# Kernel tuning notes

Measured on AMD Instinct MI355X. Metric: run time of the kernel, lower is better.

## Reference

```python
import jax, jax.numpy as jnp
import numpy as np

B, N, C, Q, H, RATIO = 8, 8700, 256, 300, 8, 4
D = C // H
HID = C * RATIO
EPS = 1e-5


def _ln(x, w, b):
    m = jnp.mean(x, axis=-1, keepdims=True)
    v = jnp.mean((x - m) ** 2, axis=-1, keepdims=True)
    return (x - m) * jax.lax.rsqrt(v + EPS) * w + b


def setup_inputs() -> dict:
    key = jax.random.key(0)
    ks = jax.random.split(key, 8)
    s = 0.02
    return {
        "x": jax.random.normal(ks[0], (B, N, C), jnp.float32),
        # linear weights stored [in, out] (y = x @ W), no biases (qkv_bias=False, Mlp bias=False)
        "Wq": jax.random.normal(ks[1], (C, C), jnp.float32) * s,
        "Wk": jax.random.normal(ks[2], (C, C), jnp.float32) * s,
        "Wv": jax.random.normal(ks[3], (C, C), jnp.float32) * s,
        "Wp": jax.random.normal(ks[4], (C, C), jnp.float32) * s,
        "W1": jax.random.normal(ks[5], (C, HID), jnp.float32) * s,
        "W2": jax.random.normal(ks[6], (HID, C), jnp.float32) * s,
        "ln1_w": jnp.ones((C,), jnp.float32),
        "ln1_b": jnp.zeros((C,), jnp.float32),
        "ln2_w": jnp.ones((C,), jnp.float32),
        "ln2_b": jnp.zeros((C,), jnp.float32),
        "gamma1": jnp.ones((C,), jnp.float32),
        "gamma2": jnp.ones((C,), jnp.float32),
    }


def reference(x, Wq, Wk, Wv, Wp, W1, W2, ln1_w, ln1_b, ln2_w, ln2_b, gamma1, gamma2):
    scale = D ** -0.5
    xn = _ln(x, ln1_w, ln1_b)                       # [B,N,C]
    # SAQAttn: queries only from the first Q tokens; keys/values from all N tokens
    q = (xn[:, :Q] @ Wq).reshape(B, Q, H, D) * scale  # [B,Q,H,D]
    k = (xn @ Wk).reshape(B, N, H, D)
    v = (xn @ Wv).reshape(B, N, H, D)
    attn = jax.nn.softmax(jnp.einsum('bqhd,bnhd->bhqn', q, k), axis=-1)  # [B,H,Q,N]
    x_det = jnp.einsum('bhqn,bnhd->bqhd', attn, v).reshape(B, Q, C) @ Wp  # [B,Q,C]
    # residual with layer-scale gamma1; context tokens pass normed features through
    x_attn = jnp.concatenate([x_det, xn[:, Q:]], axis=1)
    x = x + gamma1 * x_attn
    # tokens_norm=False: norm2 only on query tokens
    x = jnp.concatenate([_ln(x[:, :Q], ln2_w, ln2_b), x[:, Q:]], axis=1)
    # MLP on query tokens with layer-scale gamma2 (exact GELU, as nn.GELU default)
    det = gamma2 * (jax.nn.gelu(x[:, :Q] @ W1, approximate=False) @ W2)
    # faithful to source: x_res + cat([det, x[:,Q:]]) doubles the context tokens
    return x + jnp.concatenate([det, x[:, Q:]], axis=1)
```

## Files before the change

kernel.cpp:

```cpp
#include <hip/hip_runtime.h>

#define BB 8
#define NN 8700
#define CC 256
#define QQ 300
#define HH 8
#define DD 32
#define HIDN 1024
#define NSPLIT 16
#define TSTR (NSPLIT * 64)
#define KSLACK 1536

typedef unsigned short u16;
typedef __attribute__((ext_vector_type(8))) short short8;
typedef __attribute__((ext_vector_type(4))) float f32x4;

#define MFMA16(a, b, c) __builtin_amdgcn_mfma_f32_16x16x32_bf16((a), (b), (c), 0, 0, 0)

__device__ __forceinline__ u16 f2bu(float f) {
    unsigned int u = __builtin_bit_cast(unsigned int, f);
    u += 0x7fffu + ((u >> 16) & 1u);
    return (u16)(u >> 16);
}
__device__ __forceinline__ unsigned int cvtpk(float lo, float hi) {
    unsigned int r;
    asm("v_cvt_pk_bf16_f32 %0, %1, %2" : "=v"(r) : "v"(lo), "v"(hi));
    return r;
}

__global__ __launch_bounds__(256)
void wprep_all(const float* __restrict__ Wq, const float* __restrict__ Wk,
               const float* __restrict__ Wv, const float* __restrict__ Wp,
               const float* __restrict__ W1, const float* __restrict__ W2,
               u16* __restrict__ dst, float qscale)
{
    int e = blockIdx.x * 256 + threadIdx.x;
    float v;
    if (e < 65536)       { int i = e;          int n = i >> 8, k = i & 255;   v = Wq[k * 256 + n] * qscale; }
    else if (e < 131072) { int i = e - 65536;  int n = i >> 8, k = i & 255;   v = Wk[k * 256 + n]; }
    else if (e < 196608) { int i = e - 131072; int n = i >> 8, k = i & 255;   v = Wv[k * 256 + n]; }
    else if (e < 262144) { int i = e - 196608; int n = i >> 8, k = i & 255;   v = Wp[k * 256 + n]; }
    else if (e < 524288) { int i = e - 262144; int n = i >> 8, k = i & 255;   v = W1[k * 1024 + n]; }
    else                 { int i = e - 524288; int n = i >> 10, k = i & 1023; v = W2[k * 256 + n]; }
    dst[e] = f2bu(v);
}

__global__ __launch_bounds__(256)
void ln1_k(const float* __restrict__ x, const float* __restrict__ w,
           const float* __restrict__ bv, const float* __restrict__ g1,
           u16* __restrict__ xn, float* __restrict__ out)
{
    int row = blockIdx.x * 4 + (threadIdx.x >> 6);
    int l = threadIdx.x & 63;
    size_t base = (size_t)row * CC + l * 4;
    float4 xv = *reinterpret_cast<const float4*>(x + base);
    float s  = xv.x + xv.y + xv.z + xv.w;
    float s2 = xv.x * xv.x + xv.y * xv.y + xv.z * xv.z + xv.w * xv.w;
#pragma unroll
    for (int m = 1; m < 64; m <<= 1) {
        s  += __shfl_xor(s,  m, 64);
        s2 += __shfl_xor(s2, m, 64);
    }
    float mean = s * (1.0f / CC);
    float rs = rsqrtf(s2 * (1.0f / CC) - mean * mean + 1e-5f);
    float4 wv = *reinterpret_cast<const float4*>(w  + l * 4);
    float4 bb = *reinterpret_cast<const float4*>(bv + l * 4);
    float n0 = (xv.x - mean) * rs * wv.x + bb.x;
    float n1 = (xv.y - mean) * rs * wv.y + bb.y;
    float n2 = (xv.z - mean) * rs * wv.z + bb.z;
    float n3 = (xv.w - mean) * rs * wv.w + bb.w;
    ushort4 u; u.x = f2bu(n0); u.y = f2bu(n1); u.z = f2bu(n2); u.w = f2bu(n3);
    *reinterpret_cast<ushort4*>(xn + base) = u;
    int n = row % NN;
    if (n >= QQ) {
        float4 gv = *reinterpret_cast<const float4*>(g1 + l * 4);
        float4 o;
        o.x = 2.0f * (xv.x + gv.x * n0);
        o.y = 2.0f * (xv.y + gv.y * n1);
        o.z = 2.0f * (xv.z + gv.z * n2);
        o.w = 2.0f * (xv.w + gv.w * n3);
        *reinterpret_cast<float4*>(out + base) = o;
    }
}

__global__ __launch_bounds__(256)
void ln2_k(const float* __restrict__ x, const float* __restrict__ pd,
           const float* __restrict__ g1, const float* __restrict__ w,
           const float* __restrict__ bv, float* __restrict__ xqf, u16* __restrict__ xqb)
{
    int r = blockIdx.x * 4 + (threadIdx.x >> 6);
    int l = threadIdx.x & 63;
    int b = r / QQ, n = r - b * QQ;
    size_t xoff = ((size_t)b * NN + n) * CC + l * 4;
    size_t roff = (size_t)r * CC + l * 4;
    float4 xv = *reinterpret_cast<const float4*>(x + xoff);
    float4 pv = *reinterpret_cast<const float4*>(pd + roff);
    float4 gv = *reinterpret_cast<const float4*>(g1 + l * 4);
    float x0 = xv.x + gv.x * pv.x;
    float x1 = xv.y + gv.y * pv.y;
    float x2 = xv.z + gv.z * pv.z;
    float x3 = xv.w + gv.w * pv.w;
    float s  = x0 + x1 + x2 + x3;
    float s2 = x0 * x0 + x1 * x1 + x2 * x2 + x3 * x3;
#pragma unroll
    for (int m = 1; m < 64; m <<= 1) {
        s  += __shfl_xor(s,  m, 64);
        s2 += __shfl_xor(s2, m, 64);
    }
    float mean = s * (1.0f / CC);
    float rs = rsqrtf(s2 * (1.0f / CC) - mean * mean + 1e-5f);
    float4 wv = *reinterpret_cast<const float4*>(w  + l * 4);
    float4 bb = *reinterpret_cast<const float4*>(bv + l * 4);
    float n0 = (x0 - mean) * rs * wv.x + bb.x;
    float n1 = (x1 - mean) * rs * wv.y + bb.y;
    float n2 = (x2 - mean) * rs * wv.z + bb.z;
    float n3 = (x3 - mean) * rs * wv.w + bb.w;
    float4 o; o.x = n0; o.y = n1; o.z = n2; o.w = n3;
    *reinterpret_cast<float4*>(xqf + roff) = o;
    ushort4 u; u.x = f2bu(n0); u.y = f2bu(n1); u.z = f2bu(n2); u.w = f2bu(n3);
    *reinterpret_cast<ushort4*>(xqb + roff) = u;
}

template<int EPI, int MT>
__global__ __launch_bounds__(256)
void gemm_k(const u16* __restrict__ A, const u16* __restrict__ WT,
            u16* __restrict__ Cb, u16* __restrict__ Cb2, float* __restrict__ Cf,
            const float* __restrict__ basep, const float* __restrict__ gvec,
            float* __restrict__ outp,
            int M, int K, int ldC, int rpb, int bstr)
{
    constexpr int NM = MT / 16;
    const int w = threadIdx.x >> 6, l = threadIdx.x & 63;
    const int l15 = l & 15, kg = l >> 4;
    const int rowbase = blockIdx.x * MT;
    const int colbase = blockIdx.y * 256 + w * 64;
    const short8 z8 = {0, 0, 0, 0, 0, 0, 0, 0};
    const f32x4 fz = {0.f, 0.f, 0.f, 0.f};

    const u16* ap[NM]; bool av[NM];
#pragma unroll
    for (int mi = 0; mi < NM; mi++) {
        int r = rowbase + mi * 16 + l15;
        av[mi] = (r < M);
        int rr = av[mi] ? r : 0;
        size_t ar = (size_t)(rr / rpb) * bstr + (rr % rpb);
        ap[mi] = A + ar * K + kg * 8;
    }
    const u16* bp[4];
#pragma unroll
    for (int ni = 0; ni < 4; ni++) {
        int col = colbase + ni * 16 + l15;
        bp[ni] = WT + (size_t)col * K + kg * 8;
    }
    f32x4 acc[NM][4];
#pragma unroll
    for (int mi = 0; mi < NM; mi++)
#pragma unroll
        for (int ni = 0; ni < 4; ni++) acc[mi][ni] = fz;

    for (int ks = 0; ks < K; ks += 32) {
        short8 a[NM], bfr[4];
#pragma unroll
        for (int mi = 0; mi < NM; mi++)
            a[mi] = av[mi] ? *reinterpret_cast<const short8*>(ap[mi] + ks) : z8;
#pragma unroll
        for (int ni = 0; ni < 4; ni++)
            bfr[ni] = *reinterpret_cast<const short8*>(bp[ni] + ks);
#pragma unroll
        for (int mi = 0; mi < NM; mi++)
#pragma unroll
            for (int ni = 0; ni < 4; ni++)
                acc[mi][ni] = MFMA16(a[mi], bfr[ni], acc[mi][ni]);
    }
#pragma unroll
    for (int mi = 0; mi < NM; mi++) {
#pragma unroll
        for (int j = 0; j < 4; j++) {
            int r = rowbase + mi * 16 + kg * 4 + j;
            if (r >= M) continue;
#pragma unroll
            for (int ni = 0; ni < 4; ni++) {
                int col = colbase + ni * 16 + l15;
                float v = acc[mi][ni][j];
                if (EPI == 0) {
                    if (col < CC) Cb[(size_t)r * ldC + col] = f2bu(v);
                    else          Cb2[(size_t)r * ldC + (col - CC)] = f2bu(v);
                } else if (EPI == 1) {
                    float gl = 0.5f * v * (1.0f + erff(v * 0.70710678118654752f));
                    Cb[(size_t)r * ldC + col] = f2bu(gl);
                } else if (EPI == 2) {
                    Cf[(size_t)r * ldC + col] = v;
                } else {
                    float res = basep[(size_t)r * CC + col] + gvec[col] * v;
                    size_t orow = (size_t)(r / QQ) * NN + (r % QQ);
                    outp[orow * CC + col] = res;
                }
            }
        }
    }
}

__global__ __launch_bounds__(256)
void attn_k(const u16* __restrict__ qm, const u16* __restrict__ km,
            const u16* __restrict__ vm, float* __restrict__ Op,
            float* __restrict__ lp)
{
    __shared__ u16 vt[2][32 * 64];
    __shared__ u16 plds[4][2][16 * 64];

    const int bx = blockIdx.x;
    const int split = bx >> 6;
    const int rem = bx & 63;
    const int h = rem >> 3, b = rem & 7;
    const int bh = b * HH + h;
    const int tid = threadIdx.x;
    const int w = tid >> 6, l = tid & 63;
    const int l15 = l & 15, kg = l >> 4;
    const int tstart = split * 64;
    const int nt = (NN - tstart + TSTR - 1) / TSTR;

    const f32x4 fz = {0.f, 0.f, 0.f, 0.f};
    const short os = (short)0x3F80;
    const short8 ones = {os, os, os, os, os, os, os, os};

    const u16* kbase = km + (size_t)b * NN * CC + h * DD;
    const u16* vbase = vm + (size_t)b * NN * CC + h * DD;
    const int vkp = (tid & 31) * 2;
    const int vdg = (tid >> 5) * 4;

    short8 qfr[5];
#pragma unroll
    for (int qf = 0; qf < 5; qf++) {
        int qrow = w * 80 + qf * 16 + l15;
        int qc = qrow < QQ ? qrow : 0;
        qfr[qf] = *reinterpret_cast<const short8*>(qm + ((size_t)(b * QQ + qc) * CC + h * DD + kg * 8));
    }

    f32x4 o[2][5]; float lpart[5];
#pragma unroll
    for (int qf = 0; qf < 5; qf++) { o[0][qf] = fz; o[1][qf] = fz; lpart[qf] = 0.f; }

    short8 kf[4]; ushort4 v0r, v1r;
#pragma unroll
    for (int kb = 0; kb < 4; kb++)
        kf[kb] = *reinterpret_cast<const short8*>(kbase + (size_t)(tstart + kb * 16 + l15) * CC + kg * 8);
    v0r = *reinterpret_cast<const ushort4*>(vbase + (size_t)(tstart + vkp) * CC + vdg);
    v1r = *reinterpret_cast<const ushort4*>(vbase + (size_t)(tstart + vkp + 1) * CC + vdg);

    char* pl = (char*)plds[w];
    const int rdswz = ((l15 << 7) ^ ((l15 & 7) << 4)) + (kg << 4);
    const int wrbase = (l15 << 7) ^ ((l15 & 7) << 4);

    for (int t = 0; t < nt; ++t) {
        const int n0 = tstart + t * TSTR;
        char* vtb = (char*)vt[t & 1];
#pragma unroll
        for (int i = 0; i < 4; i++) {
            int row = vdg + i;
            unsigned int pk2 = (unsigned int)v0r[i] | ((unsigned int)v1r[i] << 16);
            int byteo = ((row << 7) + (vkp << 1)) ^ ((row & 7) << 4);
            *reinterpret_cast<unsigned int*>(vtb + byteo) = pk2;
        }
        __syncthreads();

        short8 kfn[4]; ushort4 v0n, v1n;
        { const int n0n = n0 + TSTR;
#pragma unroll
          for (int kb = 0; kb < 4; kb++)
              kfn[kb] = *reinterpret_cast<const short8*>(kbase + (size_t)(n0n + kb * 16 + l15) * CC + kg * 8);
          v0n = *reinterpret_cast<const ushort4*>(vbase + (size_t)(n0n + vkp) * CC + vdg);
          v1n = *reinterpret_cast<const ushort4*>(vbase + (size_t)(n0n + vkp + 1) * CC + vdg); }

        short8 va[2][2];
#pragma unroll
        for (int ks = 0; ks < 2; ks++)
#pragma unroll
            for (int dg = 0; dg < 2; dg++) {
                int row = dg * 16 + l15;
                int byteo = ((row << 7) + 64 * ks + 16 * kg) ^ ((row & 7) << 4);
                va[ks][dg] = *reinterpret_cast<const short8*>(vtb + byteo);
            }

        const bool tail = (n0 + 64 > NN);

#pragma unroll
        for (int qf = 0; qf < 5; qf++) {
            short8 bp0, bp1;
            if (qf > 0) {
                const char* plr = pl + (((qf - 1) & 1) << 11);
                bp0 = *reinterpret_cast<const short8*>(plr + rdswz);
                bp1 = *reinterpret_cast<const short8*>(plr + rdswz + 64);
            }
            f32x4 s[4];
            __builtin_amdgcn_s_setprio(1);
#pragma unroll
            for (int kb = 0; kb < 4; kb++)
                s[kb] = MFMA16(kf[kb], qfr[qf], fz);
            __builtin_amdgcn_s_setprio(0);
            char* plw = pl + ((qf & 1) << 11);
#pragma unroll
            for (int kb = 0; kb < 4; kb++) {
                float p0 = exp2f(s[kb][0]);
                float p1 = exp2f(s[kb][1]);
                float p2 = exp2f(s[kb][2]);
                float p3 = exp2f(s[kb][3]);
                if (tail) {
                    int kbase2 = n0 + 16 * kb + 4 * kg;
                    if (kbase2 + 0 >= NN) p0 = 0.f;
                    if (kbase2 + 1 >= NN) p1 = 0.f;
                    if (kbase2 + 2 >= NN) p2 = 0.f;
                    if (kbase2 + 3 >= NN) p3 = 0.f;
                }
                int byte0 = wrbase + ((16 * kb + 4 * kg) << 1);
                *reinterpret_cast<unsigned int*>(plw + byte0)     = cvtpk(p0, p1);
                *reinterpret_cast<unsigned int*>(plw + byte0 + 4) = cvtpk(p2, p3);
            }
            if (qf > 0) {
                __builtin_amdgcn_s_setprio(1);
                o[0][qf - 1] = MFMA16(va[0][0], bp0, o[0][qf - 1]);
                o[1][qf - 1] = MFMA16(va[0][1], bp0, o[1][qf - 1]);
                o[0][qf - 1] = MFMA16(va[1][0], bp1, o[0][qf - 1]);
                o[1][qf - 1] = MFMA16(va[1][1], bp1, o[1][qf - 1]);
                f32x4 tsum = MFMA16(ones, bp0, fz);
                tsum = MFMA16(ones, bp1, tsum);
                __builtin_amdgcn_s_setprio(0);
                lpart[qf - 1] += tsum[0];
            }
        }
        {
            const char* plr = pl + 0;
            short8 bp0 = *reinterpret_cast<const short8*>(plr + rdswz);
            short8 bp1 = *reinterpret_cast<const short8*>(plr + rdswz + 64);
            __builtin_amdgcn_s_setprio(1);
            o[0][4] = MFMA16(va[0][0], bp0, o[0][4]);
            o[1][4] = MFMA16(va[0][1], bp0, o[1][4]);
            o[0][4] = MFMA16(va[1][0], bp1, o[0][4]);
            o[1][4] = MFMA16(va[1][1], bp1, o[1][4]);
            f32x4 tsum = MFMA16(ones, bp0, fz);
            tsum = MFMA16(ones, bp1, tsum);
            __builtin_amdgcn_s_setprio(0);
            lpart[4] += tsum[0];
        }
#pragma unroll
        for (int kb = 0; kb < 4; kb++) kf[kb] = kfn[kb];
        v0r = v0n; v1r = v1n;
    }

    size_t pb = (size_t)(split * 64 + bh) * QQ;
#pragma unroll
    for (int qf = 0; qf < 5; qf++) {
        int q = w * 80 + qf * 16 + l15;
        if (q >= QQ) continue;
        size_t pr = pb + q;
        if (kg == 0) lp[pr] = lpart[qf];
        *reinterpret_cast<f32x4*>(Op + pr * DD + kg * 4)      = o[0][qf];
        *reinterpret_cast<f32x4*>(Op + pr * DD + 16 + kg * 4) = o[1][qf];
    }
}

__global__ __launch_bounds__(256)
void comb_k(const float* __restrict__ Op, const float* __restrict__ lp, u16* __restrict__ ao)
{
    int g = blockIdx.x * 256 + threadIdx.x;
    int d4 = (g & 7) * 4;
    int row = g >> 3;
    int bh = row / QQ, qq = row - bh * QQ;
    int b = bh >> 3, h = bh & 7;
    float L = 0.f, a0 = 0.f, a1 = 0.f, a2 = 0.f, a3 = 0.f;
#pragma unroll
    for (int s = 0; s < NSPLIT; s++) {
        size_t pr = (size_t)(s * 64 + bh) * QQ + qq;
        L += lp[pr];
        float4 ov = *reinterpret_cast<const float4*>(Op + pr * DD + d4);
        a0 += ov.x; a1 += ov.y; a2 += ov.z; a3 += ov.w;
    }
    float inv = 1.0f / L;
    ushort4 u;
    u.x = f2bu(a0 * inv); u.y = f2bu(a1 * inv); u.z = f2bu(a2 * inv); u.w = f2bu(a3 * inv);
    *reinterpret_cast<ushort4*>(ao + ((size_t)(b * QQ + qq) * CC + h * DD + d4)) = u;
}

extern "C" void kernel_launch(void* const* d_in, const int* in_sizes, int n_in,
                              void* d_out, int out_size, void* d_ws, size_t ws_size,
                              hipStream_t stream)
{
    (void)in_sizes; (void)n_in; (void)out_size; (void)ws_size;
    const float* x    = (const float*)d_in[0];
    const float* Wq   = (const float*)d_in[1];
    const float* Wk   = (const float*)d_in[2];
    const float* Wv   = (const float*)d_in[3];
    const float* Wp   = (const float*)d_in[4];
    const float* W1   = (const float*)d_in[5];
    const float* W2   = (const float*)d_in[6];
    const float* ln1w = (const float*)d_in[7];
    const float* ln1b = (const float*)d_in[8];
    const float* ln2w = (const float*)d_in[9];
    const float* ln2b = (const float*)d_in[10];
    const float* g1   = (const float*)d_in[11];
    const float* g2   = (const float*)d_in[12];
    float* out = (float*)d_out;

    char* p = (char*)d_ws;
    auto alloc = [&](size_t bytes) { char* r = p; p += (bytes + 255) & ~(size_t)255; return r; };

    const size_t MKV = (size_t)BB * NN;
    const size_t MQ  = (size_t)BB * QQ;

    u16* WqT  = (u16*)alloc((size_t)CC * CC * 2);
    u16* WkvT = (u16*)alloc((size_t)CC * CC * 2 * 2);
    u16* WpT  = (u16*)alloc((size_t)CC * CC * 2);
    u16* W1T  = (u16*)alloc((size_t)CC * HIDN * 2);
    u16* W2T  = (u16*)alloc((size_t)HIDN * CC * 2);
    u16* xn   = (u16*)alloc(MKV * CC * 2);
    u16* kbf  = (u16*)alloc((MKV + KSLACK) * CC * 2);
    u16* vbf  = (u16*)alloc((MKV + KSLACK) * CC * 2);
    u16* qbf  = (u16*)alloc(MQ * CC * 2);
    u16* aob  = (u16*)alloc(MQ * CC * 2);
    u16* xqb  = (u16*)alloc(MQ * CC * 2);
    u16* h1   = (u16*)alloc(MQ * HIDN * 2);
    float* pd  = (float*)alloc(MQ * CC * 4);
    float* xqf = (float*)alloc(MQ * CC * 4);
    float* Op  = (float*)alloc((size_t)NSPLIT * 64 * QQ * DD * 4);
    float* lp  = (float*)alloc((size_t)NSPLIT * 64 * QQ * 4);

    const float qscale = 0.17677669529663687f * 1.4426950408889634f;

    wprep_all<<<3072, 256, 0, stream>>>(Wq, Wk, Wv, Wp, W1, W2, WqT, qscale);

    ln1_k<<<(int)(MKV / 4), 256, 0, stream>>>(x, ln1w, ln1b, g1, xn, out);

    gemm_k<0, 64><<<dim3(1088, 2), 256, 0, stream>>>(xn, WkvT, kbf, vbf, nullptr, nullptr, nullptr, nullptr,
                                                     (int)MKV, CC, CC, (int)MKV, 0);
    gemm_k<0, 16><<<dim3(150, 1), 256, 0, stream>>>(xn, WqT, qbf, nullptr, nullptr, nullptr, nullptr, nullptr,
                                                    (int)MQ, CC, CC, QQ, NN);

    attn_k<<<64 * NSPLIT, 256, 0, stream>>>(qbf, kbf, vbf, Op, lp);
    comb_k<<<(int)(MQ * 8 / 256), 256, 0, stream>>>(Op, lp, aob);

    gemm_k<2, 16><<<dim3(150, 1), 256, 0, stream>>>(aob, WpT, nullptr, nullptr, pd, nullptr, nullptr, nullptr,
                                                    (int)MQ, CC, CC, (int)MQ, 0);
    ln2_k<<<(int)(MQ / 4), 256, 0, stream>>>(x, pd, g1, ln2w, ln2b, xqf, xqb);

    gemm_k<1, 16><<<dim3(150, 4), 256, 0, stream>>>(xqb, W1T, h1, nullptr, nullptr, nullptr, nullptr, nullptr,
                                                    (int)MQ, CC, HIDN, (int)MQ, 0);
    gemm_k<3, 16><<<dim3(150, 1), 256, 0, stream>>>(h1, W2T, nullptr, nullptr, nullptr, xqf, g2, out,
                                                    (int)MQ, HIDN, CC, (int)MQ, 0);
}
```

Baseline: 247.7 us.

## Add dedicated KV projection GEMM staging A tile in swizzled LDS

```diff
diff --git a/kernel.cpp b/kernel.cpp
--- a/kernel.cpp
+++ b/kernel.cpp
@@ -119,6 +119,82 @@
     *reinterpret_cast<float4*>(xqf + roff) = o;
     ushort4 u; u.x = f2bu(n0); u.y = f2bu(n1); u.z = f2bu(n2); u.w = f2bu(n3);
     *reinterpret_cast<ushort4*>(xqb + roff) = u;
+}
+
+__global__ __launch_bounds__(512)
+void gemm_kv(const u16* __restrict__ A, const u16* __restrict__ WT,
+             u16* __restrict__ Cb, u16* __restrict__ Cb2, int M)
+{
+    __shared__ u16 alds[64 * 256];
+    const int tid = threadIdx.x;
+    const int w = tid >> 6, l = tid & 63;
+    const int l15 = l & 15, kg = l >> 4;
+    const int rowbase = blockIdx.x * 64;
+    const f32x4 fz = {0.f, 0.f, 0.f, 0.f};
+
+    {
+        const char* gb = (const char*)(A + (size_t)rowbase * CC);
+        char* lb = (char*)alds;
+#pragma unroll
+        for (int j = 0; j < 4; j++) {
+            int o = tid * 64 + j * 16;
+            short8 v = *reinterpret_cast<const short8*>(gb + o);
+            int d = o ^ (((o >> 9) & 7) << 4);
+            *reinterpret_cast<short8*>(lb + d) = v;
+        }
+    }
+    __syncthreads();
+
+    const int colbase = w * 64;
+    const u16* bp[4];
+#pragma unroll
+    for (int ni = 0; ni < 4; ni++)
+        bp[ni] = WT + (size_t)(colbase + ni * 16 + l15) * CC + kg * 8;
+
+    f32x4 acc[4][4];
+#pragma unroll
+    for (int mi = 0; mi < 4; mi++)
+#pragma unroll
+        for (int ni = 0; ni < 4; ni++) acc[mi][ni] = fz;
+
+    const char* lb = (const char*)alds;
+    const int sw = (l15 & 7) << 4;
+    int abase[4];
+#pragma unroll
+    for (int mi = 0; mi < 4; mi++) abase[mi] = (mi * 16 + l15) << 9;
+
+#pragma unroll
+    for (int ks = 0; ks < 8; ks++) {
+        const int koff = ((ks * 64) + (kg * 16)) ^ sw;
+        short8 a[4], bfr[4];
+#pragma unroll
+        for (int mi = 0; mi < 4; mi++)
+            a[mi] = *reinterpret_cast<const short8*>(lb + abase[mi] + koff);
+#pragma unroll
+        for (int ni = 0; ni < 4; ni++)
+            bfr[ni] = *reinterpret_cast<const short8*>(bp[ni] + ks * 32);
+#pragma unroll
+        for (int mi = 0; mi < 4; mi++)
+#pragma unroll
+            for (int ni = 0; ni < 4; ni++)
+                acc[mi][ni] = MFMA16(a[mi], bfr[ni], acc[mi][ni]);
+    }
+
+#pragma unroll
+    for (int mi = 0; mi < 4; mi++) {
+#pragma unroll
+        for (int j = 0; j < 4; j++) {
+            int r = rowbase + mi * 16 + kg * 4 + j;
+            if (r >= M) continue;
+#pragma unroll
+            for (int ni = 0; ni < 4; ni++) {
+                int col = colbase + ni * 16 + l15;
+                float v = acc[mi][ni][j];
+                if (col < CC) Cb[(size_t)r * CC + col] = f2bu(v);
+                else          Cb2[(size_t)r * CC + (col - CC)] = f2bu(v);
+            }
+        }
+    }
 }
 
 template<int EPI, int MT>
@@ -411,7 +487,7 @@
     u16* WpT  = (u16*)alloc((size_t)CC * CC * 2);
     u16* W1T  = (u16*)alloc((size_t)CC * HIDN * 2);
     u16* W2T  = (u16*)alloc((size_t)HIDN * CC * 2);
-    u16* xn   = (u16*)alloc(MKV * CC * 2);
+    u16* xn   = (u16*)alloc((MKV + 64) * CC * 2);
     u16* kbf  = (u16*)alloc((MKV + KSLACK) * CC * 2);
     u16* vbf  = (u16*)alloc((MKV + KSLACK) * CC * 2);
     u16* qbf  = (u16*)alloc(MQ * CC * 2);
@@ -429,8 +505,7 @@
 
     ln1_k<<<(int)(MKV / 4), 256, 0, stream>>>(x, ln1w, ln1b, g1, xn, out);
 
-    gemm_k<0, 64><<<dim3(1088, 2), 256, 0, stream>>>(xn, WkvT, kbf, vbf, nullptr, nullptr, nullptr, nullptr,
-                                                     (int)MKV, CC, CC, (int)MKV, 0);
+    gemm_kv<<<1088, 512, 0, stream>>>(xn, WkvT, kbf, vbf, (int)MKV);
     gemm_k<0, 16><<<dim3(150, 1), 256, 0, stream>>>(xn, WqT, qbf, nullptr, nullptr, nullptr, nullptr, nullptr,
                                                     (int)MQ, CC, CC, QQ, NN);
 
```

Result: faster. 225.0 us (-9.2%).
